# Kernel tuning notes

Measured on AMD Instinct MI355X. Metric: run time of the kernel, lower is better.

Reference implementation:

```python
import jax, jax.numpy as jnp
import numpy as np

T, B, V, H = 256, 256, 512, 1024


def setup_inputs() -> dict:
    key = jax.random.key(0)
    k1, k2, k3, k4 = jax.random.split(key, 4)
    # lecun_normal-like scaling for stability
    return {
        "inputs": jax.random.normal(k1, (T, B, V), dtype=jnp.float32),
        "W_xh": jax.random.normal(k2, (V, H), dtype=jnp.float32) / np.sqrt(V),
        "W_hh": jax.random.normal(k3, (H, H), dtype=jnp.float32) / np.sqrt(H),
        "b_h": jnp.zeros((H,), dtype=jnp.float32),
        "W_dense": jax.random.normal(k4, (H, V), dtype=jnp.float32) / np.sqrt(H),
        "b_dense": jnp.zeros((V,), dtype=jnp.float32),
    }


def reference(inputs, W_xh, W_hh, b_h, W_dense, b_dense):
    # Pre-compute the input projection for all timesteps (one big GEMM).
    xh = jnp.einsum("tbv,vh->tbh", inputs, W_xh) + b_h  # [T, B, H]

    def step(h, x_t):
        h_new = jnp.tanh(x_t + jnp.matmul(h, W_hh))
        return h_new, h_new

    h0 = jnp.zeros((inputs.shape[1], W_hh.shape[0]), dtype=inputs.dtype)
    state, hs = jax.lax.scan(step, h0, xh)  # hs: [T, B, H]

    outputs = jnp.einsum("tbh,hv->tbv", hs, W_dense) + b_dense  # [T, B, V]
    return outputs, state
```

## Files before the change

### kernel.cpp

```cpp
#include <hip/hip_runtime.h>


#define T_STEPS 256
#define B_SZ    256
#define V_SZ    512
#define H_SZ    1024
#define BH      (B_SZ * H_SZ)
#define M1      (T_STEPS * B_SZ)

typedef __attribute__((ext_vector_type(8))) short bf16x8;
typedef __attribute__((ext_vector_type(4))) float f32x4;

__device__ inline unsigned short bf16_rne(float f) {
    unsigned u = __float_as_uint(f);
    u += 0x7fffu + ((u >> 16) & 1u);
    return (unsigned short)(u >> 16);
}

__global__ __launch_bounds__(256, 4)
void gemm_f32_xh(const float* __restrict__ A, const float* __restrict__ Bw,
                 const float* __restrict__ bias, float* __restrict__ C)
{
    __shared__ __align__(16) float As[16][128];
    __shared__ __align__(16) float Bs[16][128];
    const int tid = threadIdx.x;
    const int tx = tid & 15, ty = tid >> 4;
    const int r0 = blockIdx.y * 128, c0 = blockIdx.x * 128;
    const int ar = tid >> 1, ak = (tid & 1) * 8;
    const int bk = tid >> 4, bc = (tid & 15) * 8;

    float acc[8][8] = {};

    for (int kc = 0; kc < V_SZ; kc += 16) {
        const float* ap = A + (size_t)(r0 + ar) * V_SZ + kc + ak;
        float4 a0 = ((const float4*)ap)[0];
        float4 a1 = ((const float4*)ap)[1];
        const float* bp = Bw + (size_t)(kc + bk) * H_SZ + c0 + bc;
        float4 b0 = ((const float4*)bp)[0];
        float4 b1 = ((const float4*)bp)[1];
        __syncthreads();
        As[ak + 0][ar] = a0.x; As[ak + 1][ar] = a0.y;
        As[ak + 2][ar] = a0.z; As[ak + 3][ar] = a0.w;
        As[ak + 4][ar] = a1.x; As[ak + 5][ar] = a1.y;
        As[ak + 6][ar] = a1.z; As[ak + 7][ar] = a1.w;
        *(float4*)&Bs[bk][bc]     = b0;
        *(float4*)&Bs[bk][bc + 4] = b1;
        __syncthreads();
#pragma unroll
        for (int kk = 0; kk < 16; ++kk) {
            float ra[8], rb[8];
            *(float4*)(ra)     = *(const float4*)&As[kk][ty * 8];
            *(float4*)(ra + 4) = *(const float4*)&As[kk][ty * 8 + 4];
            *(float4*)(rb)     = *(const float4*)&Bs[kk][tx * 8];
            *(float4*)(rb + 4) = *(const float4*)&Bs[kk][tx * 8 + 4];
#pragma unroll
            for (int i = 0; i < 8; ++i)
#pragma unroll
                for (int j = 0; j < 8; ++j)
                    acc[i][j] += ra[i] * rb[j];
        }
    }

    float4 bv0 = *(const float4*)(bias + c0 + tx * 8);
    float4 bv1 = *(const float4*)(bias + c0 + tx * 8 + 4);
#pragma unroll
    for (int i = 0; i < 8; ++i) {
        float* cp = C + (size_t)(r0 + ty * 8 + i) * H_SZ + c0 + tx * 8;
        float4 o0, o1;
        o0.x = acc[i][0] + bv0.x; o0.y = acc[i][1] + bv0.y;
        o0.z = acc[i][2] + bv0.z; o0.w = acc[i][3] + bv0.w;
        o1.x = acc[i][4] + bv1.x; o1.y = acc[i][5] + bv1.y;
        o1.z = acc[i][6] + bv1.z; o1.w = acc[i][7] + bv1.w;
        ((float4*)cp)[0] = o0;
        ((float4*)cp)[1] = o1;
    }
}

__global__ __launch_bounds__(512, 2)
void scan_gemm(const float* __restrict__ Hprev, const float* __restrict__ Whh,
               float* __restrict__ P)
{
    __shared__ __align__(16) float As[16][68];
    __shared__ __align__(16) float Bs[16][128];
    const int tid = threadIdx.x;
    const int tx = tid & 31, ty = tid >> 5;
    const int c0 = blockIdx.x * 128;
    const int r0 = blockIdx.y * 64;
    const int k0 = blockIdx.z * 128;
    const int ar = tid >> 3, ak = (tid & 7) * 2;
    const int bk = tid >> 5, bc = (tid & 31) * 4;

    float acc[4][4] = {};

    for (int kc = 0; kc < 128; kc += 16) {
        float2 a2 = *(const float2*)(Hprev + (size_t)(r0 + ar) * H_SZ + k0 + kc + ak);
        float4 b4 = *(const float4*)(Whh + (size_t)(k0 + kc + bk) * H_SZ + c0 + bc);
        __syncthreads();
        As[ak][ar]     = a2.x;
        As[ak + 1][ar] = a2.y;
        *(float4*)&Bs[bk][bc] = b4;
        __syncthreads();
#pragma unroll
        for (int kk = 0; kk < 16; ++kk) {
            float4 ra = *(const float4*)&As[kk][ty * 4];
            float4 rb = *(const float4*)&Bs[kk][tx * 4];
            acc[0][0] += ra.x * rb.x; acc[0][1] += ra.x * rb.y;
            acc[0][2] += ra.x * rb.z; acc[0][3] += ra.x * rb.w;
            acc[1][0] += ra.y * rb.x; acc[1][1] += ra.y * rb.y;
            acc[1][2] += ra.y * rb.z; acc[1][3] += ra.y * rb.w;
            acc[2][0] += ra.z * rb.x; acc[2][1] += ra.z * rb.y;
            acc[2][2] += ra.z * rb.z; acc[2][3] += ra.z * rb.w;
            acc[3][0] += ra.w * rb.x; acc[3][1] += ra.w * rb.y;
            acc[3][2] += ra.w * rb.z; acc[3][3] += ra.w * rb.w;
        }
    }

    float* pp = P + (size_t)blockIdx.z * BH;
#pragma unroll
    for (int i = 0; i < 4; ++i) {
        float4 o; o.x = acc[i][0]; o.y = acc[i][1]; o.z = acc[i][2]; o.w = acc[i][3];
        *(float4*)(pp + (size_t)(r0 + ty * 4 + i) * H_SZ + c0 + tx * 4) = o;
    }
}

__global__ __launch_bounds__(256)
void scan_reduce(const float* __restrict__ P, float* __restrict__ XH)
{
    int i = (blockIdx.x * 256 + threadIdx.x) * 4;
    float4 s = *(const float4*)(XH + i);
#pragma unroll
    for (int ks = 0; ks < 8; ++ks) {
        float4 p = *(const float4*)(P + (size_t)ks * BH + i);
        s.x += p.x; s.y += p.y; s.z += p.z; s.w += p.w;
    }
    float4 o;
    o.x = tanhf(s.x); o.y = tanhf(s.y); o.z = tanhf(s.z); o.w = tanhf(s.w);
    *(float4*)(XH + i) = o;
}

__global__ __launch_bounds__(256)
void tanh_inplace(float* __restrict__ X)
{
    int i = (blockIdx.x * 256 + threadIdx.x) * 4;
    float4 x = *(float4*)(X + i);
    float4 o;
    o.x = tanhf(x.x); o.y = tanhf(x.y); o.z = tanhf(x.z); o.w = tanhf(x.w);
    *(float4*)(X + i) = o;
}

__global__ __launch_bounds__(256)
void cvt_wdense(const float* __restrict__ Wd, unsigned short* __restrict__ WdT)
{
    __shared__ float tile[64][65];
    const int tid = threadIdx.x;
    const int kt = blockIdx.x * 64, nt = blockIdx.y * 64;
    const int kr = tid >> 2, nc = (tid & 3) * 16;
#pragma unroll
    for (int i = 0; i < 4; ++i) {
        float4 v = *(const float4*)(Wd + (size_t)(kt + kr) * V_SZ + nt + nc + i * 4);
        tile[kr][nc + i * 4 + 0] = v.x;
        tile[kr][nc + i * 4 + 1] = v.y;
        tile[kr][nc + i * 4 + 2] = v.z;
        tile[kr][nc + i * 4 + 3] = v.w;
    }
    __syncthreads();
    const int nr = tid >> 2, kc = (tid & 3) * 16;
    unsigned words[8];
#pragma unroll
    for (int j = 0; j < 8; ++j) {
        unsigned short lo = bf16_rne(tile[kc + 2 * j][nr]);
        unsigned short hi = bf16_rne(tile[kc + 2 * j + 1][nr]);
        words[j] = (unsigned)lo | ((unsigned)hi << 16);
    }
    unsigned* wp = (unsigned*)(WdT + (size_t)(nt + nr) * H_SZ + kt + kc);
    ((uint4*)wp)[0] = make_uint4(words[0], words[1], words[2], words[3]);
    ((uint4*)wp)[1] = make_uint4(words[4], words[5], words[6], words[7]);
}

__global__ __launch_bounds__(256, 2)
void gemm_out_mfma(const float* __restrict__ hs, const unsigned short* __restrict__ WdT,
                   const float* __restrict__ bias, float* __restrict__ out)
{
    __shared__ __align__(16) short As[128 * 40];
    __shared__ __align__(16) short Bs[128 * 32];
    const int tid = threadIdx.x;
    const int lane = tid & 63;
    const int w = tid >> 6;
    const int r0 = blockIdx.y * 128, c0 = blockIdx.x * 128;
    const int rw = (w >> 1) * 64, cw = (w & 1) * 64;

    const int s_row = tid & 127;
    const int s_kh  = tid >> 7;
    const int b_n   = tid >> 2;
    const int b_q   = tid & 3;

    f32x4 acc[4][4];
#pragma unroll
    for (int i = 0; i < 4; ++i)
#pragma unroll
        for (int j = 0; j < 4; ++j)
            acc[i][j] = (f32x4){0.f, 0.f, 0.f, 0.f};

    const int l15 = lane & 15, l16 = lane >> 4;

    for (int kc = 0; kc < H_SZ; kc += 32) {
        const float* ap = hs + (size_t)(r0 + s_row) * H_SZ + kc + s_kh * 16;
        float4 a0 = ((const float4*)ap)[0];
        float4 a1 = ((const float4*)ap)[1];
        float4 a2 = ((const float4*)ap)[2];
        float4 a3 = ((const float4*)ap)[3];
        unsigned pk[8];
        pk[0] = __builtin_amdgcn_perm(__float_as_uint(a0.y), __float_as_uint(a0.x), 0x07060302u);
        pk[1] = __builtin_amdgcn_perm(__float_as_uint(a0.w), __float_as_uint(a0.z), 0x07060302u);
        pk[2] = __builtin_amdgcn_perm(__float_as_uint(a1.y), __float_as_uint(a1.x), 0x07060302u);
        pk[3] = __builtin_amdgcn_perm(__float_as_uint(a1.w), __float_as_uint(a1.z), 0x07060302u);
        pk[4] = __builtin_amdgcn_perm(__float_as_uint(a2.y), __float_as_uint(a2.x), 0x07060302u);
        pk[5] = __builtin_amdgcn_perm(__float_as_uint(a2.w), __float_as_uint(a2.z), 0x07060302u);
        pk[6] = __builtin_amdgcn_perm(__float_as_uint(a3.y), __float_as_uint(a3.x), 0x07060302u);
        pk[7] = __builtin_amdgcn_perm(__float_as_uint(a3.w), __float_as_uint(a3.z), 0x07060302u);
        bf16x8 bld0 = *(const bf16x8*)(WdT + (size_t)(c0 + b_n) * H_SZ + kc + b_q * 8);
        bf16x8 bld1 = *(const bf16x8*)(WdT + (size_t)(c0 + b_n + 64) * H_SZ + kc + b_q * 8);
        __syncthreads();
        ((uint4*)&As[s_row * 40 + s_kh * 16])[0] = make_uint4(pk[0], pk[1], pk[2], pk[3]);
        ((uint4*)&As[s_row * 40 + s_kh * 16 + 8])[0] = make_uint4(pk[4], pk[5], pk[6], pk[7]);
        *(bf16x8*)(&Bs[b_n * 32 + b_q * 8]) = bld0;
        *(bf16x8*)(&Bs[(b_n + 64) * 32 + b_q * 8]) = bld1;
        __syncthreads();

        bf16x8 af[4], bf[4];
#pragma unroll
        for (int mi = 0; mi < 4; ++mi)
            af[mi] = *(const bf16x8*)(&As[(rw + mi * 16 + l15) * 40 + l16 * 8]);
#pragma unroll
        for (int ni = 0; ni < 4; ++ni)
            bf[ni] = *(const bf16x8*)(&Bs[(cw + ni * 16 + l15) * 32 + l16 * 8]);
#pragma unroll
        for (int mi = 0; mi < 4; ++mi)
#pragma unroll
            for (int ni = 0; ni < 4; ++ni)
                acc[mi][ni] = __builtin_amdgcn_mfma_f32_16x16x32_bf16(
                    af[mi], bf[ni], acc[mi][ni], 0, 0, 0);
    }

#pragma unroll
    for (int ni = 0; ni < 4; ++ni) {
        const int col = c0 + cw + ni * 16 + l15;
        const float bv = bias[col];
#pragma unroll
        for (int mi = 0; mi < 4; ++mi) {
            const int rowb = r0 + rw + mi * 16 + l16 * 4;
#pragma unroll
            for (int r = 0; r < 4; ++r)
                out[(size_t)(rowb + r) * V_SZ + col] = acc[mi][ni][r] + bv;
        }
    }
}

__global__ __launch_bounds__(256)
void copy_f4(const float* __restrict__ src, float* __restrict__ dst)
{
    int i = blockIdx.x * 256 + threadIdx.x;
    ((float4*)dst)[i] = ((const float4*)src)[i];
}

extern "C" void kernel_launch(void* const* d_in, const int* in_sizes, int n_in,
                              void* d_out, int out_size, void* d_ws, size_t ws_size,
                              hipStream_t stream)
{
    const float* inputs  = (const float*)d_in[0];
    const float* W_xh    = (const float*)d_in[1];
    const float* W_hh    = (const float*)d_in[2];
    const float* b_h     = (const float*)d_in[3];
    const float* W_dense = (const float*)d_in[4];
    const float* b_dense = (const float*)d_in[5];
    float* out = (float*)d_out;

    float* buf = (float*)d_ws;
    float* P   = out;
    unsigned short* WdT = (unsigned short*)(out + (size_t)M1 * V_SZ);

    cvt_wdense<<<dim3(H_SZ / 64, V_SZ / 64), 256, 0, stream>>>(W_dense, WdT);

    gemm_f32_xh<<<dim3(H_SZ / 128, M1 / 128), 256, 0, stream>>>(
        inputs, W_xh, b_h, buf);

    tanh_inplace<<<dim3(BH / 1024), 256, 0, stream>>>(buf);

    for (int t = 1; t < T_STEPS; ++t) {
        scan_gemm<<<dim3(8, 4, 8), 512, 0, stream>>>(
            buf + (size_t)(t - 1) * BH, W_hh, P);
        scan_reduce<<<dim3(BH / 1024), 256, 0, stream>>>(P, buf + (size_t)t * BH);
    }

    gemm_out_mfma<<<dim3(V_SZ / 128, M1 / 128), 256, 0, stream>>>(
        buf, WdT, b_dense, out);

    copy_f4<<<dim3(BH / 1024), 256, 0, stream>>>(
        buf + (size_t)(T_STEPS - 1) * BH, out + (size_t)M1 * V_SZ);
}
```

Before: 5.462 ms.

## Replace per-step scan launches with persistent cooperative kernel and software barriers

The 255 pairs of per-timestep GEMM and reduce launches are replaced by a single persistent cooperative kernel with 256 blocks. Each block keeps a 64x256 slice of W_hh resident in LDS, does its split-K partial product, and reduces across its four K-split peers through global memory. The timesteps are ordered by atomic-counter barriers: one per output tile and one per row group. This removes launch overhead and the repeated reloads of W_hh, but it relies on all blocks being co-resident and on a spin-wait with a bounded timeout that could silently break correctness.

```diff
diff --git a/kernel.cpp b/kernel.cpp
--- a/kernel.cpp
+++ b/kernel.cpp
@@ -7,6 +7,12 @@
 #define H_SZ    1024
 #define BH      (B_SZ * H_SZ)
 #define M1      (T_STEPS * B_SZ)
+
+#define SC_BLOCKS  256
+#define SC_THREADS 256
+#define WS_STRIDE  260
+#define AS_STRIDE  40
+#define SPIN_MAX   (1 << 17)
 
 typedef __attribute__((ext_vector_type(8))) short bf16x8;
 typedef __attribute__((ext_vector_type(4))) float f32x4;
@@ -76,68 +82,6 @@
     }
 }
 
-__global__ __launch_bounds__(512, 2)
-void scan_gemm(const float* __restrict__ Hprev, const float* __restrict__ Whh,
-               float* __restrict__ P)
-{
-    __shared__ __align__(16) float As[16][68];
-    __shared__ __align__(16) float Bs[16][128];
-    const int tid = threadIdx.x;
-    const int tx = tid & 31, ty = tid >> 5;
-    const int c0 = blockIdx.x * 128;
-    const int r0 = blockIdx.y * 64;
-    const int k0 = blockIdx.z * 128;
-    const int ar = tid >> 3, ak = (tid & 7) * 2;
-    const int bk = tid >> 5, bc = (tid & 31) * 4;
-
-    float acc[4][4] = {};
-
-    for (int kc = 0; kc < 128; kc += 16) {
-        float2 a2 = *(const float2*)(Hprev + (size_t)(r0 + ar) * H_SZ + k0 + kc + ak);
-        float4 b4 = *(const float4*)(Whh + (size_t)(k0 + kc + bk) * H_SZ + c0 + bc);
-        __syncthreads();
-        As[ak][ar]     = a2.x;
-        As[ak + 1][ar] = a2.y;
-        *(float4*)&Bs[bk][bc] = b4;
-        __syncthreads();
-#pragma unroll
-        for (int kk = 0; kk < 16; ++kk) {
-            float4 ra = *(const float4*)&As[kk][ty * 4];
-            float4 rb = *(const float4*)&Bs[kk][tx * 4];
-            acc[0][0] += ra.x * rb.x; acc[0][1] += ra.x * rb.y;
-            acc[0][2] += ra.x * rb.z; acc[0][3] += ra.x * rb.w;
-            acc[1][0] += ra.y * rb.x; acc[1][1] += ra.y * rb.y;
-            acc[1][2] += ra.y * rb.z; acc[1][3] += ra.y * rb.w;
-            acc[2][0] += ra.z * rb.x; acc[2][1] += ra.z * rb.y;
-            acc[2][2] += ra.z * rb.z; acc[2][3] += ra.z * rb.w;
-            acc[3][0] += ra.w * rb.x; acc[3][1] += ra.w * rb.y;
-            acc[3][2] += ra.w * rb.z; acc[3][3] += ra.w * rb.w;
-        }
-    }
-
-    float* pp = P + (size_t)blockIdx.z * BH;
-#pragma unroll
-    for (int i = 0; i < 4; ++i) {
-        float4 o; o.x = acc[i][0]; o.y = acc[i][1]; o.z = acc[i][2]; o.w = acc[i][3];
-        *(float4*)(pp + (size_t)(r0 + ty * 4 + i) * H_SZ + c0 + tx * 4) = o;
-    }
-}
-
-__global__ __launch_bounds__(256)
-void scan_reduce(const float* __restrict__ P, float* __restrict__ XH)
-{
-    int i = (blockIdx.x * 256 + threadIdx.x) * 4;
-    float4 s = *(const float4*)(XH + i);
-#pragma unroll
-    for (int ks = 0; ks < 8; ++ks) {
-        float4 p = *(const float4*)(P + (size_t)ks * BH + i);
-        s.x += p.x; s.y += p.y; s.z += p.z; s.w += p.w;
-    }
-    float4 o;
-    o.x = tanhf(s.x); o.y = tanhf(s.y); o.z = tanhf(s.z); o.w = tanhf(s.w);
-    *(float4*)(XH + i) = o;
-}
-
 __global__ __launch_bounds__(256)
 void tanh_inplace(float* __restrict__ X)
 {
@@ -146,6 +90,163 @@
     float4 o;
     o.x = tanhf(x.x); o.y = tanhf(x.y); o.z = tanhf(x.z); o.w = tanhf(x.w);
     *(float4*)(X + i) = o;
+}
+
+__global__ __launch_bounds__(256)
+void init_bars(int* __restrict__ bar)
+{
+    bar[blockIdx.x * 256 + threadIdx.x] = 0;
+}
+
+__device__ __forceinline__ void bar_sync(int* __restrict__ bar, int id, int n, int t)
+{
+    __syncthreads();
+    if (threadIdx.x == 0) {
+        int* cnt = bar + id * 64;
+        int* gen = bar + id * 64 + 32;
+        __threadfence();
+        int old = __hip_atomic_fetch_add(cnt, 1, __ATOMIC_ACQ_REL, __HIP_MEMORY_SCOPE_AGENT);
+        if (old == n - 1) {
+            __hip_atomic_store(cnt, 0, __ATOMIC_RELAXED, __HIP_MEMORY_SCOPE_AGENT);
+            __hip_atomic_store(gen, t, __ATOMIC_RELEASE, __HIP_MEMORY_SCOPE_AGENT);
+        } else {
+            int spin = 0;
+            while (__hip_atomic_load(gen, __ATOMIC_ACQUIRE, __HIP_MEMORY_SCOPE_AGENT) < t) {
+                __builtin_amdgcn_s_sleep(2);
+                if (++spin > SPIN_MAX) break;
+            }
+        }
+        __threadfence();
+    }
+    __syncthreads();
+}
+
+__global__ __launch_bounds__(SC_THREADS, 1)
+void scan_persistent(float* __restrict__ buf, const float* __restrict__ Whh,
+                     float* __restrict__ P, int* __restrict__ bar)
+{
+    __shared__ __align__(16) float Ws[64 * WS_STRIDE];
+    __shared__ __align__(16) float As[2 * 64 * AS_STRIDE];
+    __shared__ __align__(16) float Rb[4 * 4096];
+
+    const int tid  = threadIdx.x;
+    const int bid  = blockIdx.x;
+    const int ks   = bid >> 6;
+    const int tile = bid & 63;
+    const int rowg = tile >> 4;
+    const int colg = tile & 15;
+    const int b0 = rowg * 64;
+    const int c0 = colg * 64;
+    const int k0 = ks * 256;
+
+    const int w  = tid >> 6;
+    const int l  = tid & 63;
+    const int lr = l >> 3;
+    const int lc = l & 7;
+
+    for (int idx = tid; idx < 64 * 256; idx += SC_THREADS) {
+        int c = idx & 63, kp = idx >> 6;
+        Ws[c * WS_STRIDE + kp] = Whh[(size_t)(k0 + kp) * H_SZ + c0 + c];
+    }
+    __syncthreads();
+
+    const int sr = tid >> 3, skq = tid & 7;
+    float* Pblk = P + (size_t)(tile * 4 + ks) * 4096;
+    const float* Ptile = P + (size_t)tile * 4 * 4096;
+
+    for (int t = 1; t < T_STEPS; ++t) {
+        const float* hprev = buf + (size_t)(t - 1) * BH;
+
+        float acc[8][8];
+#pragma unroll
+        for (int i = 0; i < 8; ++i)
+#pragma unroll
+            for (int j = 0; j < 8; ++j) acc[i][j] = 0.f;
+
+        {
+            const float* ap = hprev + (size_t)(b0 + sr) * H_SZ + k0 + skq * 4;
+            float4 v0 = *(const float4*)ap;
+            float4 v1 = *(const float4*)(ap + (size_t)32 * H_SZ);
+            *(float4*)&As[sr * AS_STRIDE + skq * 4] = v0;
+            *(float4*)&As[(sr + 32) * AS_STRIDE + skq * 4] = v1;
+        }
+        __syncthreads();
+
+        for (int ch = 0; ch < 8; ++ch) {
+            const int cb = ch & 1, nb = cb ^ 1;
+            float4 v0, v1;
+            if (ch < 7) {
+                const float* ap = hprev + (size_t)(b0 + sr) * H_SZ + k0 + (ch + 1) * 32 + skq * 4;
+                v0 = *(const float4*)ap;
+                v1 = *(const float4*)(ap + (size_t)32 * H_SZ);
+            }
+            const float* Ab = &As[cb * (64 * AS_STRIDE)];
+#pragma unroll
+            for (int qi = 0; qi < 2; ++qi) {
+                const int kk = (w + qi * 4) * 4;
+                const int kp = ch * 32 + kk;
+                float4 a[8], b[8];
+#pragma unroll
+                for (int i = 0; i < 8; ++i)
+                    a[i] = *(const float4*)&Ab[(8 * i + lr) * AS_STRIDE + kk];
+#pragma unroll
+                for (int j = 0; j < 8; ++j)
+                    b[j] = *(const float4*)&Ws[(8 * j + lc) * WS_STRIDE + kp];
+#pragma unroll
+                for (int i = 0; i < 8; ++i)
+#pragma unroll
+                    for (int j = 0; j < 8; ++j)
+                        acc[i][j] += a[i].x * b[j].x + a[i].y * b[j].y
+                                   + a[i].z * b[j].z + a[i].w * b[j].w;
+            }
+            if (ch < 7) {
+                *(float4*)&As[nb * (64 * AS_STRIDE) + sr * AS_STRIDE + skq * 4] = v0;
+                *(float4*)&As[nb * (64 * AS_STRIDE) + (sr + 32) * AS_STRIDE + skq * 4] = v1;
+                __syncthreads();
+            }
+        }
+
+#pragma unroll
+        for (int i = 0; i < 8; ++i)
+#pragma unroll
+            for (int j = 0; j < 8; ++j)
+                Rb[w * 4096 + (i * 8 + j) * 64 + l] = acc[i][j];
+        __syncthreads();
+#pragma unroll
+        for (int u = 0; u < 4; ++u) {
+            int idx = u * 1024 + tid * 4;
+            float4 s0 = *(const float4*)&Rb[idx];
+            float4 s1 = *(const float4*)&Rb[4096 + idx];
+            float4 s2 = *(const float4*)&Rb[8192 + idx];
+            float4 s3 = *(const float4*)&Rb[12288 + idx];
+            float4 s;
+            s.x = (s0.x + s1.x) + (s2.x + s3.x);
+            s.y = (s0.y + s1.y) + (s2.y + s3.y);
+            s.z = (s0.z + s1.z) + (s2.z + s3.z);
+            s.w = (s0.w + s1.w) + (s2.w + s3.w);
+            *(float4*)&Pblk[idx] = s;
+        }
+
+        bar_sync(bar, tile, 4, t);
+
+        float* ht = buf + (size_t)t * BH;
+#pragma unroll
+        for (int m = 0; m < 4; ++m) {
+            int g = w * 4 + m;
+            int i = 2 * ks + (g >> 3);
+            int j = g & 7;
+            int gi = (i * 8 + j) * 64 + l;
+            float s = (Ptile[gi] + Ptile[4096 + gi])
+                    + (Ptile[8192 + gi] + Ptile[12288 + gi]);
+            int row = b0 + 8 * i + lr;
+            int col = c0 + 8 * j + lc;
+            float* hp = ht + (size_t)row * H_SZ + col;
+            s += *hp;
+            *hp = tanhf(s);
+        }
+
+        if (t < T_STEPS - 1) bar_sync(bar, 64 + rowg, 64, t);
+    }
 }
 
 __global__ __launch_bounds__(256)
@@ -277,6 +378,7 @@
 
     float* buf = (float*)d_ws;
     float* P   = out;
+    int*   bar = (int*)(out + 1310720);
     unsigned short* WdT = (unsigned short*)(out + (size_t)M1 * V_SZ);
 
     cvt_wdense<<<dim3(H_SZ / 64, V_SZ / 64), 256, 0, stream>>>(W_dense, WdT);
@@ -286,10 +388,20 @@
 
     tanh_inplace<<<dim3(BH / 1024), 256, 0, stream>>>(buf);
 
-    for (int t = 1; t < T_STEPS; ++t) {
-        scan_gemm<<<dim3(8, 4, 8), 512, 0, stream>>>(
-            buf + (size_t)(t - 1) * BH, W_hh, P);
-        scan_reduce<<<dim3(BH / 1024), 256, 0, stream>>>(P, buf + (size_t)t * BH);
+    init_bars<<<dim3(32), 256, 0, stream>>>(bar);
+    {
+        void* args[4];
+        args[0] = (void*)&buf;
+        args[1] = (void*)&W_hh;
+        args[2] = (void*)&P;
+        args[3] = (void*)&bar;
+        hipError_t e = hipLaunchCooperativeKernel((void*)scan_persistent,
+                                                  dim3(SC_BLOCKS), dim3(SC_THREADS),
+                                                  args, 0, stream);
+        if (e != hipSuccess) {
+            scan_persistent<<<dim3(SC_BLOCKS), dim3(SC_THREADS), 0, stream>>>(
+                buf, W_hh, P, bar);
+        }
     }
 
     gemm_out_mfma<<<dim3(V_SZ / 128, M1 / 128), 256, 0, stream>>>(
```

Result: slower. 20.77 ms (+280.4%).
